# Kernel tuning notes

Hardware: AMD Instinct MI355X
Metric: run time of the kernel (lower is better)

The kernel has to match this reference:

```python
import jax, jax.numpy as jnp
import numpy as np
import math

DT = 1.0
BETA = 15.0
TAU0 = 3.0
THRESHOLD = 0.25


def setup_inputs() -> dict:
    key = jax.random.key(0)
    B, F, L = 64, 256, 2048
    I = jax.random.normal(key, (B, F, L), dtype=jnp.float32)
    raw0 = math.log(math.expm1(TAU0))
    raw_tau = jnp.full((F,), raw0, dtype=jnp.float32)
    thr = jnp.float32(THRESHOLD)
    return {"I": I, "raw_tau": raw_tau, "thr": thr}


def reference(I, raw_tau, thr):
    B, F, L = I.shape
    tau = jax.nn.softplus(raw_tau) + 1e-4          # [F]
    alpha = jnp.exp(-DT / tau).astype(I.dtype)      # [F] decay per filter

    def step(v, I_t):
        # v: [B, F], I_t: [B, F]
        v_pre = alpha * v + (1.0 - alpha) * I_t
        z = BETA * (v_pre - thr)
        s = (v_pre >= thr).astype(I.dtype)
        v_new = v_pre * (1.0 - s)                   # hard reset on spike
        return v_new, (z, s)

    I_time = jnp.moveaxis(I, -1, 0)                 # [L, B, F]
    v0 = jnp.zeros((B, F), dtype=I.dtype)
    _, (z_hist, s_hist) = jax.lax.scan(step, v0, I_time)
    # back to [B, F, L]
    return jnp.moveaxis(z_hist, 0, -1), jnp.moveaxis(s_hist, 0, -1)
```

## Files before the change

### kernel.cpp

```cpp
#include <hip/hip_runtime.h>
#include <cmath>

#define LIF_L 2048
#define LIF_F 256
#define LIF_B 64
#define LIF_BF (LIF_B * LIF_F)
#define TT 64
#define NTILE (LIF_L / TT)
#define STR 65

__global__ __launch_bounds__(64) void lif_scan_kernel(
    const float* __restrict__ I, const float* __restrict__ raw_tau,
    const float* __restrict__ thr_p, float* __restrict__ out) {
#pragma clang fp contract(off)
  __shared__ float ldsI[64 * STR];
  __shared__ float ldsZ[64 * STR];
  __shared__ float ldsS[64 * STR];

  const int lane = threadIdx.x;
  const int cbase = blockIdx.x * 64;
  const int q = lane >> 4;
  const int m = lane & 15;

  const int f = (cbase + lane) & (LIF_F - 1);
  const double rt = (double)raw_tau[f];
  const double sp = (rt > 0.0) ? (rt + log1p(exp(-rt))) : log1p(exp(rt));
  const float alpha = (float)exp(-1.0 / (sp + 1e-4));
  const float oma = 1.0f - alpha;
  const float thr = thr_p[0];
  const float beta = 15.0f;

  const float4* __restrict__ Ip = (const float4*)I;
  float4* __restrict__ Zp = (float4*)out;
  float4* __restrict__ Sp = (float4*)(out + (size_t)LIF_BF * LIF_L);

  float v = 0.0f;
  float4 inbuf[16];

#pragma unroll
  for (int k = 0; k < 16; ++k) {
    const int row = 4 * k + q;
    inbuf[k] = Ip[(size_t)(cbase + row) * (LIF_L / 4) + m];
  }

  for (int tile = 0; tile < NTILE; ++tile) {
#pragma unroll
    for (int k = 0; k < 16; ++k) {
      const int row = 4 * k + q;
      float* p = &ldsI[row * STR + 4 * m];
      p[0] = inbuf[k].x; p[1] = inbuf[k].y; p[2] = inbuf[k].z; p[3] = inbuf[k].w;
    }
    const int tn = (tile + 1 < NTILE) ? tile + 1 : tile;
#pragma unroll
    for (int k = 0; k < 16; ++k) {
      const int row = 4 * k + q;
      inbuf[k] = Ip[(size_t)(cbase + row) * (LIF_L / 4) + tn * (TT / 4) + m];
    }
    __builtin_amdgcn_wave_barrier();

    float* rowI = &ldsI[lane * STR];
    float* rowZ = &ldsZ[lane * STR];
    float* rowS = &ldsS[lane * STR];
#pragma unroll 8
    for (int t = 0; t < TT; ++t) {
      const float in = rowI[t];
      const float vpre = alpha * v + oma * in;
      rowZ[t] = beta * (vpre - thr);
      rowS[t] = (vpre >= thr) ? 1.0f : 0.0f;
      v = (vpre >= thr) ? 0.0f : vpre;
    }
    __builtin_amdgcn_wave_barrier();

#pragma unroll
    for (int k = 0; k < 16; ++k) {
      const int row = 4 * k + q;
      const size_t oidx = (size_t)(cbase + row) * (LIF_L / 4) + tile * (TT / 4) + m;
      const float* pz = &ldsZ[row * STR + 4 * m];
      float4 zv = {pz[0], pz[1], pz[2], pz[3]};
      Zp[oidx] = zv;
      const float* ps = &ldsS[row * STR + 4 * m];
      float4 sv = {ps[0], ps[1], ps[2], ps[3]};
      Sp[oidx] = sv;
    }
    __builtin_amdgcn_wave_barrier();
  }
}

extern "C" void kernel_launch(void* const* d_in, const int* in_sizes, int n_in,
                              void* d_out, int out_size, void* d_ws,
                              size_t ws_size, hipStream_t stream) {
  const float* I = (const float*)d_in[0];
  const float* raw_tau = (const float*)d_in[1];
  const float* thr = (const float*)d_in[2];
  float* out = (float*)d_out;
  dim3 grid(LIF_BF / 64), block(64);
  lif_scan_kernel<<<grid, block, 0, stream>>>(I, raw_tau, thr, out);
}
```

Before: 384.4 us.

## Warp-specialize LIF scan into compute and producer/consumer waves with double-buffered LDS

Each block now has two waves. Wave 0 runs the serial recurrence in place on a double-buffered LDS tile, writing z over the input. Wave 1 streams the next tile's global loads into LDS and writes out the previous tile's z and s, deriving s from the sign of z. This aims to hide global memory latency behind the sequential scan and to cut LDS traffic and footprint. In exchange it adds a __syncthreads per tile and relies on z >= 0 matching vpre >= thr exactly.

```diff
diff --git a/kernel.cpp b/kernel.cpp
--- a/kernel.cpp
+++ b/kernel.cpp
@@ -9,80 +9,109 @@
 #define NTILE (LIF_L / TT)
 #define STR 65
 
-__global__ __launch_bounds__(64) void lif_scan_kernel(
+__global__ __launch_bounds__(128) void lif_scan_kernel(
     const float* __restrict__ I, const float* __restrict__ raw_tau,
     const float* __restrict__ thr_p, float* __restrict__ out) {
 #pragma clang fp contract(off)
-  __shared__ float ldsI[64 * STR];
-  __shared__ float ldsZ[64 * STR];
-  __shared__ float ldsS[64 * STR];
+  __shared__ float buf[2][64 * STR];
 
-  const int lane = threadIdx.x;
+  const int tid = threadIdx.x;
+  const int wid = tid >> 6;
+  const int lane = tid & 63;
   const int cbase = blockIdx.x * 64;
-  const int q = lane >> 4;
-  const int m = lane & 15;
-
-  const int f = (cbase + lane) & (LIF_F - 1);
-  const double rt = (double)raw_tau[f];
-  const double sp = (rt > 0.0) ? (rt + log1p(exp(-rt))) : log1p(exp(rt));
-  const float alpha = (float)exp(-1.0 / (sp + 1e-4));
-  const float oma = 1.0f - alpha;
-  const float thr = thr_p[0];
-  const float beta = 15.0f;
 
   const float4* __restrict__ Ip = (const float4*)I;
   float4* __restrict__ Zp = (float4*)out;
   float4* __restrict__ Sp = (float4*)(out + (size_t)LIF_BF * LIF_L);
 
+  const int q = lane >> 4;
+  const int m = lane & 15;
+
+  float alpha = 0.0f, oma = 0.0f, thr = 0.0f;
   float v = 0.0f;
   float4 inbuf[16];
 
+  if (wid == 0) {
+    const int f = (cbase + lane) & (LIF_F - 1);
+    const double rt = (double)raw_tau[f];
+    const double sp = (rt > 0.0) ? (rt + log1p(exp(-rt))) : log1p(exp(rt));
+    alpha = (float)exp(-1.0 / (sp + 1e-4));
+    oma = 1.0f - alpha;
+    thr = thr_p[0];
+  } else {
 #pragma unroll
-  for (int k = 0; k < 16; ++k) {
-    const int row = 4 * k + q;
-    inbuf[k] = Ip[(size_t)(cbase + row) * (LIF_L / 4) + m];
-  }
-
-  for (int tile = 0; tile < NTILE; ++tile) {
+    for (int k = 0; k < 16; ++k)
+      inbuf[k] = Ip[(size_t)(cbase + 4 * k + q) * (LIF_L / 4) + m];
 #pragma unroll
     for (int k = 0; k < 16; ++k) {
       const int row = 4 * k + q;
-      float* p = &ldsI[row * STR + 4 * m];
+      float* p = &buf[0][row * STR + 4 * m];
       p[0] = inbuf[k].x; p[1] = inbuf[k].y; p[2] = inbuf[k].z; p[3] = inbuf[k].w;
     }
-    const int tn = (tile + 1 < NTILE) ? tile + 1 : tile;
+#pragma unroll
+    for (int k = 0; k < 16; ++k)
+      inbuf[k] = Ip[(size_t)(cbase + 4 * k + q) * (LIF_L / 4) + (TT / 4) + m];
+  }
+  __syncthreads();
+
+  for (int i = 0; i < NTILE; ++i) {
+    if (wid == 1) {
+      if (i >= 1) {
+        const float* zb = buf[(i - 1) & 1];
+#pragma unroll
+        for (int k = 0; k < 16; ++k) {
+          const int row = 4 * k + q;
+          const float* pz = &zb[row * STR + 4 * m];
+          float4 zv = {pz[0], pz[1], pz[2], pz[3]};
+          float4 sv = {zv.x >= 0.0f ? 1.0f : 0.0f, zv.y >= 0.0f ? 1.0f : 0.0f,
+                       zv.z >= 0.0f ? 1.0f : 0.0f, zv.w >= 0.0f ? 1.0f : 0.0f};
+          const size_t oidx =
+              (size_t)(cbase + row) * (LIF_L / 4) + (size_t)(i - 1) * (TT / 4) + m;
+          Zp[oidx] = zv;
+          Sp[oidx] = sv;
+        }
+      }
+      if (i + 1 < NTILE) {
+#pragma unroll
+        for (int k = 0; k < 16; ++k) {
+          const int row = 4 * k + q;
+          float* p = &buf[(i + 1) & 1][row * STR + 4 * m];
+          p[0] = inbuf[k].x; p[1] = inbuf[k].y; p[2] = inbuf[k].z; p[3] = inbuf[k].w;
+        }
+      }
+      if (i + 2 < NTILE) {
+#pragma unroll
+        for (int k = 0; k < 16; ++k)
+          inbuf[k] = Ip[(size_t)(cbase + 4 * k + q) * (LIF_L / 4) +
+                        (size_t)(i + 2) * (TT / 4) + m];
+      }
+    } else {
+      float* rowv = &buf[i & 1][lane * STR];
+#pragma unroll 16
+      for (int t = 0; t < TT; ++t) {
+        const float in = rowv[t];
+        const float vpre = alpha * v + oma * in;
+        rowv[t] = 15.0f * (vpre - thr);
+        v = (vpre >= thr) ? 0.0f : vpre;
+      }
+    }
+    __syncthreads();
+  }
+
+  if (wid == 1) {
+    const float* zb = buf[(NTILE - 1) & 1];
 #pragma unroll
     for (int k = 0; k < 16; ++k) {
       const int row = 4 * k + q;
-      inbuf[k] = Ip[(size_t)(cbase + row) * (LIF_L / 4) + tn * (TT / 4) + m];
-    }
-    __builtin_amdgcn_wave_barrier();
-
-    float* rowI = &ldsI[lane * STR];
-    float* rowZ = &ldsZ[lane * STR];
-    float* rowS = &ldsS[lane * STR];
-#pragma unroll 8
-    for (int t = 0; t < TT; ++t) {
-      const float in = rowI[t];
-      const float vpre = alpha * v + oma * in;
-      rowZ[t] = beta * (vpre - thr);
-      rowS[t] = (vpre >= thr) ? 1.0f : 0.0f;
-      v = (vpre >= thr) ? 0.0f : vpre;
-    }
-    __builtin_amdgcn_wave_barrier();
-
-#pragma unroll
-    for (int k = 0; k < 16; ++k) {
-      const int row = 4 * k + q;
-      const size_t oidx = (size_t)(cbase + row) * (LIF_L / 4) + tile * (TT / 4) + m;
-      const float* pz = &ldsZ[row * STR + 4 * m];
+      const float* pz = &zb[row * STR + 4 * m];
       float4 zv = {pz[0], pz[1], pz[2], pz[3]};
+      float4 sv = {zv.x >= 0.0f ? 1.0f : 0.0f, zv.y >= 0.0f ? 1.0f : 0.0f,
+                   zv.z >= 0.0f ? 1.0f : 0.0f, zv.w >= 0.0f ? 1.0f : 0.0f};
+      const size_t oidx =
+          (size_t)(cbase + row) * (LIF_L / 4) + (size_t)(NTILE - 1) * (TT / 4) + m;
       Zp[oidx] = zv;
-      const float* ps = &ldsS[row * STR + 4 * m];
-      float4 sv = {ps[0], ps[1], ps[2], ps[3]};
       Sp[oidx] = sv;
     }
-    __builtin_amdgcn_wave_barrier();
   }
 }
 
@@ -93,6 +122,6 @@
   const float* raw_tau = (const float*)d_in[1];
   const float* thr = (const float*)d_in[2];
   float* out = (float*)d_out;
-  dim3 grid(LIF_BF / 64), block(64);
+  dim3 grid(LIF_BF / 64), block(128);
   lif_scan_kernel<<<grid, block, 0, stream>>>(I, raw_tau, thr, out);
 }
```

Measured after the change: 382.3 us. About the same (-0.5%).
